# Optimization experiments

Measured on AMD Instinct MI355X. Metric: run time of the kernel, lower is better.

## Reference

```python
import jax, jax.numpy as jnp
import numpy as np

B, T, F, U = 64, 512, 1024, 64


def setup_inputs() -> dict:
    key = jax.random.key(0)
    ks = jax.random.split(key, 6)
    return {
        "x": jax.random.normal(ks[0], (B, T, F), dtype=jnp.float32),
        "kernel": jax.random.normal(ks[1], (F, U), dtype=jnp.float32) * (1.0 / np.sqrt(F)),
        "bias": jax.random.normal(ks[2], (U,), dtype=jnp.float32) * 0.02,
        "chain_kernel": jax.random.normal(ks[3], (U, U), dtype=jnp.float32) * 0.1,
        "left_boundary": jax.random.normal(ks[4], (U,), dtype=jnp.float32) * 0.1,
        "right_boundary": jax.random.normal(ks[5], (U,), dtype=jnp.float32) * 0.1,
    }


def _viterbi_decode(potentials, chain_kernel):
    # potentials: [B, T, U], chain_kernel: [U, U]
    def step(alpha, pot_t):
        # alpha: [B, U] best score ending in each tag at t-1
        scores = alpha[:, :, None] + chain_kernel[None, :, :] + pot_t[:, None, :]  # [B, U_prev, U_cur]
        return jnp.max(scores, axis=1), jnp.argmax(scores, axis=1)

    pots_t = jnp.moveaxis(potentials[:, 1:], 1, 0)  # [T-1, B, U]
    alpha_last, backptrs = jax.lax.scan(step, potentials[:, 0], pots_t)
    last_tag = jnp.argmax(alpha_last, axis=-1)  # [B]

    def back(tag, bp):
        prev = jnp.take_along_axis(bp, tag[:, None], axis=1)[:, 0]
        return prev, prev

    _, tags = jax.lax.scan(back, last_tag, backptrs, reverse=True)  # [T-1, B], positions 0..T-2
    path = jnp.concatenate([jnp.moveaxis(tags, 0, 1), last_tag[:, None]], axis=1)
    return path.astype(jnp.int32)


def reference(x, kernel, bias, chain_kernel, left_boundary, right_boundary):
    # dense projection (activation = linear)
    potentials = jnp.einsum("btf,fu->btu", x, kernel) + bias  # [B, T, U]
    # boundary energies (mask=None path: add to first/last timestep)
    potentials = potentials.at[:, 0, :].add(left_boundary)
    potentials = potentials.at[:, -1, :].add(right_boundary)
    return _viterbi_decode(potentials, chain_kernel)
```

## Files before the change

kernel.cpp:

```cpp
#include <hip/hip_runtime.h>

#define B_ 64
#define T_ 512
#define F_ 1024
#define U_ 64

__global__ __launch_bounds__(256) void crf_gemm_kernel(
    const float* __restrict__ x, const float* __restrict__ w,
    const float* __restrict__ bias, const float* __restrict__ lb,
    const float* __restrict__ rb, float* __restrict__ pot)
{
    const int tid = threadIdx.x;
    const int rt = tid >> 4;
    const int ut = tid & 15;
    const int n0 = blockIdx.x * 128;
    const int r0 = rt * 8;
    const int u0 = ut * 4;

    float acc[8][4];
#pragma unroll
    for (int i = 0; i < 8; ++i)
#pragma unroll
        for (int j = 0; j < 4; ++j) acc[i][j] = 0.f;

    const float* xbase = x + (size_t)(n0 + r0) * F_;

    for (int f4 = 0; f4 < F_ / 4; ++f4) {
        float xv[8][4];
#pragma unroll
        for (int i = 0; i < 8; ++i) {
            const float4 t4 = *reinterpret_cast<const float4*>(
                xbase + (size_t)i * F_ + f4 * 4);
            xv[i][0] = t4.x; xv[i][1] = t4.y; xv[i][2] = t4.z; xv[i][3] = t4.w;
        }
        float kv[4][4];
#pragma unroll
        for (int ff = 0; ff < 4; ++ff) {
            const float4 t4 = *reinterpret_cast<const float4*>(
                w + (size_t)(f4 * 4 + ff) * U_ + u0);
            kv[ff][0] = t4.x; kv[ff][1] = t4.y; kv[ff][2] = t4.z; kv[ff][3] = t4.w;
        }
#pragma unroll
        for (int ff = 0; ff < 4; ++ff)
#pragma unroll
            for (int i = 0; i < 8; ++i)
#pragma unroll
                for (int j = 0; j < 4; ++j)
                    acc[i][j] = fmaf(xv[i][ff], kv[ff][j], acc[i][j]);
    }

    const int t0 = n0 & (T_ - 1);
    const float4 bs4 = *reinterpret_cast<const float4*>(bias + u0);
    const float4 lb4 = *reinterpret_cast<const float4*>(lb + u0);
    const float4 rb4 = *reinterpret_cast<const float4*>(rb + u0);

#pragma unroll
    for (int i = 0; i < 8; ++i) {
        const int n = n0 + r0 + i;
        const int t = t0 + r0 + i;
        float4 o;
        o.x = acc[i][0] + bs4.x;
        o.y = acc[i][1] + bs4.y;
        o.z = acc[i][2] + bs4.z;
        o.w = acc[i][3] + bs4.w;
        if (t == 0)      { o.x += lb4.x; o.y += lb4.y; o.z += lb4.z; o.w += lb4.w; }
        if (t == T_ - 1) { o.x += rb4.x; o.y += rb4.y; o.z += rb4.z; o.w += rb4.w; }
        *reinterpret_cast<float4*>(pot + (size_t)n * U_ + u0) = o;
    }
}

__global__ __launch_bounds__(256) void crf_viterbi_kernel(
    const float* __restrict__ pot, const float* __restrict__ chain,
    int* __restrict__ path)
{
    const int b = blockIdx.x;
    const int tid = threadIdx.x;
    const int u = tid & 63;
    const int g = tid >> 6;

    __shared__ __align__(16) float alpha_s[64];
    __shared__ float pval[4][64];
    __shared__ int   pidx[4][64];
    __shared__ unsigned char bp[T_ - 1][64];

    float chain_r[16];
#pragma unroll
    for (int k = 0; k < 16; ++k)
        chain_r[k] = chain[(size_t)(g * 16 + k) * U_ + u];

    const float* potb = pot + (size_t)b * T_ * U_;

    if (g == 0) alpha_s[u] = potb[u];
    __syncthreads();

    float pc = potb[(size_t)U_ + u];

    for (int t = 1; t < T_; ++t) {
        const int tn = (t + 1 < T_) ? (t + 1) : (T_ - 1);
        const float pn = potb[(size_t)tn * U_ + u];

        const float4* a4 = reinterpret_cast<const float4*>(alpha_s);
        float best = -3.402823466e38f;
        int bidx = 0;
#pragma unroll
        for (int q = 0; q < 4; ++q) {
            const float4 av = a4[g * 4 + q];
            const float avv[4] = {av.x, av.y, av.z, av.w};
#pragma unroll
            for (int kk = 0; kk < 4; ++kk) {
                const int k = q * 4 + kk;
                const float s2 = (avv[kk] + chain_r[k]) + pc;
                if (s2 > best) { best = s2; bidx = g * 16 + k; }
            }
        }
        pval[g][u] = best;
        pidx[g][u] = bidx;
        __syncthreads();
        if (g == 0) {
            float bv = pval[0][u];
            int   bi = pidx[0][u];
#pragma unroll
            for (int j = 1; j < 4; ++j) {
                const float v = pval[j][u];
                if (v > bv) { bv = v; bi = pidx[j][u]; }
            }
            bp[t - 1][u] = (unsigned char)bi;
            alpha_s[u] = bv;
        }
        __syncthreads();
        pc = pn;
    }

    if (tid == 0) {
        float bv = alpha_s[0];
        int bi = 0;
        for (int v = 1; v < 64; ++v) {
            const float a = alpha_s[v];
            if (a > bv) { bv = a; bi = v; }
        }
        int* pb = path + (size_t)b * T_;
        int tag = bi;
        pb[T_ - 1] = tag;
        for (int t = T_ - 2; t >= 0; --t) {
            tag = bp[t][tag];
            pb[t] = tag;
        }
    }
}

extern "C" void kernel_launch(void* const* d_in, const int* in_sizes, int n_in,
                              void* d_out, int out_size, void* d_ws, size_t ws_size,
                              hipStream_t stream) {
    const float* x  = (const float*)d_in[0];
    const float* w  = (const float*)d_in[1];
    const float* bs = (const float*)d_in[2];
    const float* ck = (const float*)d_in[3];
    const float* lb = (const float*)d_in[4];
    const float* rb = (const float*)d_in[5];

    float* pot = (float*)d_ws;
    int* path  = (int*)d_out;

    crf_gemm_kernel<<<dim3(256), dim3(256), 0, stream>>>(x, w, bs, lb, rb, pot);
    crf_viterbi_kernel<<<dim3(B_), dim3(256), 0, stream>>>(pot, ck, path);
}
```

Before: 414.9 us.

## Stage weights in LDS, shrink GEMM tile, and parallelize Viterbi backtrace

The GEMM kernel now stages weight chunks in shared memory with register double-buffering of x and W, uses 64-row tiles so 512 blocks run at two blocks per CU, and prefetches the next chunk during compute. The Viterbi kernel prefetches potentials three steps ahead, replaces the sequential argmax with a tree reduction, and uses lighter LDS-only barriers. The backtrace is split into four segments: per-segment tag maps are composed first, then each segment is walked in parallel. These target the memory-bound projection and the serial latency of the recurrence and backtrace, at the cost of more LDS use and more complex control flow.

Result: no change. 413.9 us (-0.2%).

```diff
diff --git a/kernel.cpp b/kernel.cpp
--- a/kernel.cpp
+++ b/kernel.cpp
@@ -4,49 +4,106 @@
 #define T_ 512
 #define F_ 1024
 #define U_ 64
-
-__global__ __launch_bounds__(256) void crf_gemm_kernel(
+#define FK 128
+#define NCH (F_ / FK)
+
+__device__ __forceinline__ void block_barrier_lds() {
+    asm volatile("s_waitcnt lgkmcnt(0)" ::: "memory");
+    __builtin_amdgcn_s_barrier();
+    asm volatile("" ::: "memory");
+}
+
+__global__ __launch_bounds__(256, 2) void crf_gemm_kernel(
     const float* __restrict__ x, const float* __restrict__ w,
     const float* __restrict__ bias, const float* __restrict__ lb,
     const float* __restrict__ rb, float* __restrict__ pot)
 {
+    __shared__ float wlds[FK * U_];
+
     const int tid = threadIdx.x;
     const int rt = tid >> 4;
     const int ut = tid & 15;
-    const int n0 = blockIdx.x * 128;
-    const int r0 = rt * 8;
+    const int n0 = blockIdx.x * 64;
+    const int r0 = rt * 4;
     const int u0 = ut * 4;
 
-    float acc[8][4];
-#pragma unroll
-    for (int i = 0; i < 8; ++i)
+    float acc[4][4];
+#pragma unroll
+    for (int i = 0; i < 4; ++i)
 #pragma unroll
         for (int j = 0; j < 4; ++j) acc[i][j] = 0.f;
 
-    const float* xbase = x + (size_t)(n0 + r0) * F_;
-
-    for (int f4 = 0; f4 < F_ / 4; ++f4) {
-        float xv[8][4];
-#pragma unroll
-        for (int i = 0; i < 8; ++i) {
-            const float4 t4 = *reinterpret_cast<const float4*>(
-                xbase + (size_t)i * F_ + f4 * 4);
-            xv[i][0] = t4.x; xv[i][1] = t4.y; xv[i][2] = t4.z; xv[i][3] = t4.w;
-        }
-        float kv[4][4];
-#pragma unroll
-        for (int ff = 0; ff < 4; ++ff) {
-            const float4 t4 = *reinterpret_cast<const float4*>(
-                w + (size_t)(f4 * 4 + ff) * U_ + u0);
-            kv[ff][0] = t4.x; kv[ff][1] = t4.y; kv[ff][2] = t4.z; kv[ff][3] = t4.w;
-        }
-#pragma unroll
-        for (int ff = 0; ff < 4; ++ff)
-#pragma unroll
-            for (int i = 0; i < 8; ++i)
-#pragma unroll
-                for (int j = 0; j < 4; ++j)
-                    acc[i][j] = fmaf(xv[i][ff], kv[ff][j], acc[i][j]);
+    const float* xrow = x + (size_t)(n0 + r0) * F_;
+
+    float4 wst[8];
+#pragma unroll
+    for (int l = 0; l < 8; ++l)
+        wst[l] = *reinterpret_cast<const float4*>(w + (size_t)(l * 256 + tid) * 4);
+#pragma unroll
+    for (int l = 0; l < 8; ++l)
+        *reinterpret_cast<float4*>(&wlds[(l * 256 + tid) * 4]) = wst[l];
+    __syncthreads();
+
+    float4 xp0[4], xp1[4];
+#pragma unroll
+    for (int i = 0; i < 4; ++i)
+        xp0[i] = *reinterpret_cast<const float4*>(xrow + (size_t)i * F_ + 0);
+#pragma unroll
+    for (int i = 0; i < 4; ++i)
+        xp1[i] = *reinterpret_cast<const float4*>(xrow + (size_t)i * F_ + 4);
+
+    for (int c = 0; c < NCH; ++c) {
+        if (c + 1 < NCH) {
+#pragma unroll
+            for (int l = 0; l < 8; ++l)
+                wst[l] = *reinterpret_cast<const float4*>(
+                    w + (size_t)(c + 1) * (FK * U_) + (size_t)(l * 256 + tid) * 4);
+        }
+
+        float4 wc[4];
+#pragma unroll
+        for (int j = 0; j < 4; ++j)
+            wc[j] = *reinterpret_cast<const float4*>(&wlds[(0 + j) * U_ + u0]);
+
+        for (int kk = 0; kk < FK / 4; ++kk) {
+            const int kg = (c * FK + kk * 4 + 8) & (F_ - 1);
+            float4 xn[4];
+#pragma unroll
+            for (int i = 0; i < 4; ++i)
+                xn[i] = *reinterpret_cast<const float4*>(xrow + (size_t)i * F_ + kg);
+
+            float4 wn[4];
+            const int krn = (kk * 4 + 4) & (FK - 1);
+#pragma unroll
+            for (int j = 0; j < 4; ++j)
+                wn[j] = *reinterpret_cast<const float4*>(&wlds[(krn + j) * U_ + u0]);
+
+#pragma unroll
+            for (int ff = 0; ff < 4; ++ff) {
+                const float4 wf = wc[ff];
+#pragma unroll
+                for (int i = 0; i < 4; ++i) {
+                    const float xs = (ff == 0) ? xp0[i].x : (ff == 1) ? xp0[i].y
+                                   : (ff == 2) ? xp0[i].z : xp0[i].w;
+                    acc[i][0] = fmaf(xs, wf.x, acc[i][0]);
+                    acc[i][1] = fmaf(xs, wf.y, acc[i][1]);
+                    acc[i][2] = fmaf(xs, wf.z, acc[i][2]);
+                    acc[i][3] = fmaf(xs, wf.w, acc[i][3]);
+                }
+            }
+#pragma unroll
+            for (int i = 0; i < 4; ++i) { xp0[i] = xp1[i]; xp1[i] = xn[i]; }
+#pragma unroll
+            for (int j = 0; j < 4; ++j) wc[j] = wn[j];
+        }
+
+        if (c + 1 < NCH) {
+            __syncthreads();
+#pragma unroll
+            for (int l = 0; l < 8; ++l)
+                *reinterpret_cast<float4*>(&wlds[(l * 256 + tid) * 4]) = wst[l];
+            __syncthreads();
+        }
     }
 
     const int t0 = n0 & (T_ - 1);
@@ -55,7 +112,7 @@
     const float4 rb4 = *reinterpret_cast<const float4*>(rb + u0);
 
 #pragma unroll
-    for (int i = 0; i < 8; ++i) {
+    for (int i = 0; i < 4; ++i) {
         const int n = n0 + r0 + i;
         const int t = t0 + r0 + i;
         float4 o;
@@ -82,6 +139,8 @@
     __shared__ float pval[4][64];
     __shared__ int   pidx[4][64];
     __shared__ unsigned char bp[T_ - 1][64];
+    __shared__ unsigned char cmap[4][64];
+    __shared__ int es[4];
 
     float chain_r[16];
 #pragma unroll
@@ -91,59 +150,103 @@
     const float* potb = pot + (size_t)b * T_ * U_;
 
     if (g == 0) alpha_s[u] = potb[u];
-    __syncthreads();
-
-    float pc = potb[(size_t)U_ + u];
+
+    float p0 = potb[1 * U_ + u];
+    float p1 = potb[2 * U_ + u];
+    float p2 = potb[3 * U_ + u];
+    block_barrier_lds();
 
     for (int t = 1; t < T_; ++t) {
-        const int tn = (t + 1 < T_) ? (t + 1) : (T_ - 1);
-        const float pn = potb[(size_t)tn * U_ + u];
+        const int tp = (t + 3 < T_) ? (t + 3) : (T_ - 1);
+        const float pnew = potb[(size_t)tp * U_ + u];
+        const float pc = p0;
 
         const float4* a4 = reinterpret_cast<const float4*>(alpha_s);
-        float best = -3.402823466e38f;
-        int bidx = 0;
+        float s[16];
 #pragma unroll
         for (int q = 0; q < 4; ++q) {
             const float4 av = a4[g * 4 + q];
-            const float avv[4] = {av.x, av.y, av.z, av.w};
-#pragma unroll
-            for (int kk = 0; kk < 4; ++kk) {
-                const int k = q * 4 + kk;
-                const float s2 = (avv[kk] + chain_r[k]) + pc;
-                if (s2 > best) { best = s2; bidx = g * 16 + k; }
-            }
-        }
-        pval[g][u] = best;
-        pidx[g][u] = bidx;
-        __syncthreads();
+            s[q * 4 + 0] = (av.x + chain_r[q * 4 + 0]) + pc;
+            s[q * 4 + 1] = (av.y + chain_r[q * 4 + 1]) + pc;
+            s[q * 4 + 2] = (av.z + chain_r[q * 4 + 2]) + pc;
+            s[q * 4 + 3] = (av.w + chain_r[q * 4 + 3]) + pc;
+        }
+        float tv[8]; int ti[8];
+#pragma unroll
+        for (int i = 0; i < 8; ++i) {
+            const bool gt = s[2 * i + 1] > s[2 * i];
+            tv[i] = gt ? s[2 * i + 1] : s[2 * i];
+            ti[i] = gt ? 2 * i + 1 : 2 * i;
+        }
+        float uv[4]; int ui[4];
+#pragma unroll
+        for (int i = 0; i < 4; ++i) {
+            const bool gt = tv[2 * i + 1] > tv[2 * i];
+            uv[i] = gt ? tv[2 * i + 1] : tv[2 * i];
+            ui[i] = gt ? ti[2 * i + 1] : ti[2 * i];
+        }
+        const bool g0_ = uv[1] > uv[0];
+        const float w0 = g0_ ? uv[1] : uv[0];
+        const int   i0 = g0_ ? ui[1] : ui[0];
+        const bool g1_ = uv[3] > uv[2];
+        const float w1 = g1_ ? uv[3] : uv[2];
+        const int   i1 = g1_ ? ui[3] : ui[2];
+        const bool gf = w1 > w0;
+        const float bv16 = gf ? w1 : w0;
+        const int   bi16 = gf ? i1 : i0;
+
+        pval[g][u] = bv16;
+        pidx[g][u] = g * 16 + bi16;
+        block_barrier_lds();
+
         if (g == 0) {
             float bv = pval[0][u];
             int   bi = pidx[0][u];
 #pragma unroll
             for (int j = 1; j < 4; ++j) {
-                const float v = pval[j][u];
-                if (v > bv) { bv = v; bi = pidx[j][u]; }
+                const float vv = pval[j][u];
+                if (vv > bv) { bv = vv; bi = pidx[j][u]; }
             }
+            alpha_s[u] = bv;
             bp[t - 1][u] = (unsigned char)bi;
-            alpha_s[u] = bv;
-        }
-        __syncthreads();
-        pc = pn;
-    }
+        }
+        block_barrier_lds();
+
+        p0 = p1; p1 = p2; p2 = pnew;
+    }
+
+    const int r0c = g * 128;
+    const int r1c = (g == 3) ? (T_ - 1) : (g + 1) * 128;
+
+    {
+        int tag = u;
+        for (int r = r1c - 1; r >= r0c; --r) tag = bp[r][tag];
+        cmap[g][u] = (unsigned char)tag;
+    }
+    block_barrier_lds();
 
     if (tid == 0) {
-        float bv = alpha_s[0];
-        int bi = 0;
+        float bvv = alpha_s[0];
+        int bii = 0;
         for (int v = 1; v < 64; ++v) {
             const float a = alpha_s[v];
-            if (a > bv) { bv = a; bi = v; }
-        }
+            if (a > bvv) { bvv = a; bii = v; }
+        }
+        path[(size_t)b * T_ + (T_ - 1)] = bii;
+        const int e3 = bii;
+        const int e2 = cmap[3][e3];
+        const int e1 = cmap[2][e2];
+        const int e0 = cmap[1][e1];
+        es[0] = e0; es[1] = e1; es[2] = e2; es[3] = e3;
+    }
+    block_barrier_lds();
+
+    if (u == 0) {
+        int tag = es[g];
         int* pb = path + (size_t)b * T_;
-        int tag = bi;
-        pb[T_ - 1] = tag;
-        for (int t = T_ - 2; t >= 0; --t) {
-            tag = bp[t][tag];
-            pb[t] = tag;
+        for (int r = r1c - 1; r >= r0c; --r) {
+            tag = bp[r][tag];
+            pb[r] = tag;
         }
     }
 }
@@ -161,6 +264,6 @@
     float* pot = (float*)d_ws;
     int* path  = (int*)d_out;
 
-    crf_gemm_kernel<<<dim3(256), dim3(256), 0, stream>>>(x, w, bs, lb, rb, pot);
+    crf_gemm_kernel<<<dim3(B_ * T_ / 64), dim3(256), 0, stream>>>(x, w, bs, lb, rb, pot);
     crf_viterbi_kernel<<<dim3(B_), dim3(256), 0, stream>>>(pot, ck, path);
 }
```
